# Performance work log

Hardware: AMD Instinct MI355X
Metric: run time of the kernel (lower is better)

The kernel has to match this reference:

```python
import jax, jax.numpy as jnp
import numpy as np

EMBED_DIM = 1024
NUM_HEADS = 16
HEAD_DIM = EMBED_DIM // NUM_HEADS
FF_DIM = 4096
EPS = 1e-5


def layer_norm(x, gamma, beta):
    mu = jnp.mean(x, axis=-1, keepdims=True)
    var = jnp.var(x, axis=-1, keepdims=True)
    return (x - mu) * jax.lax.rsqrt(var + EPS) * gamma + beta


def setup_inputs() -> dict:
    key = jax.random.key(0)
    ks = jax.random.split(key, 10)
    B, S = 2, 2048
    sd = 1.0 / np.sqrt(EMBED_DIM)
    sf = 1.0 / np.sqrt(FF_DIM)
    return {
        "x": jax.random.normal(ks[0], (B, S, EMBED_DIM), jnp.float32),
        # grouped QKV: 3*num_heads groups, each embed_dim -> head_dim
        "Wqkv": jax.random.normal(ks[1], (3 * NUM_HEADS, EMBED_DIM, HEAD_DIM), jnp.float32) * sd,
        "bqkv": jnp.zeros((3 * NUM_HEADS, HEAD_DIM), jnp.float32),
        "Wo": jax.random.normal(ks[2], (EMBED_DIM, EMBED_DIM), jnp.float32) * sd,
        "bo": jnp.zeros((EMBED_DIM,), jnp.float32),
        "W1": jax.random.normal(ks[3], (EMBED_DIM, FF_DIM), jnp.float32) * sd,
        "b1": jnp.zeros((FF_DIM,), jnp.float32),
        "W2": jax.random.normal(ks[4], (FF_DIM, EMBED_DIM), jnp.float32) * sf,
        "b2": jnp.zeros((EMBED_DIM,), jnp.float32),
        "ln1_g": jnp.ones((EMBED_DIM,), jnp.float32),
        "ln1_b": jnp.zeros((EMBED_DIM,), jnp.float32),
        "ln2_g": jnp.ones((EMBED_DIM,), jnp.float32),
        "ln2_b": jnp.zeros((EMBED_DIM,), jnp.float32),
    }


def reference(x, Wqkv, bqkv, Wo, bo, W1, b1, W2, b2, ln1_g, ln1_b, ln2_g, ln2_b):
    B, S, D = x.shape
    normed = layer_norm(x, ln1_g, ln1_b)
    # grouped QKV projection: group g gets its own (D, head_dim) weight
    qkv = jnp.einsum('bsd,gdh->bgsh', normed, Wqkv) + bqkv[None, :, None, :]
    qkv = qkv.reshape(B, 3, NUM_HEADS, S, HEAD_DIM)
    q, k, v = qkv[:, 0], qkv[:, 1], qkv[:, 2]  # each [B, H, S, hd]
    attn = jnp.einsum('bhqd,bhkd->bhqk', q, k) / np.sqrt(HEAD_DIM)
    attn = jax.nn.softmax(attn, axis=-1)
    out = jnp.einsum('bhqk,bhkd->bhqd', attn, v)
    out = out.transpose(0, 2, 1, 3).reshape(B, S, D)
    out = out @ Wo + bo
    x = x + out
    normed2 = layer_norm(x, ln2_g, ln2_b)
    ff = jax.nn.relu(normed2 @ W1 + b1) @ W2 + b2
    return x + ff
```

## Files before the change

kernel.cpp:

```cpp
#include <hip/hip_runtime.h>
#include <stdint.h>

#define SEQ    2048
#define NB     2
#define NHEADS 16
#define HDIM   64
#define EMBED  1024
#define NROWS  (NB*SEQ)
#define QKVSZ  ((size_t)NB*NHEADS*SEQ*HDIM)

typedef __attribute__((ext_vector_type(8))) short short8;
typedef __attribute__((ext_vector_type(4))) float float4v;
typedef __attribute__((ext_vector_type(16))) float float16v;
typedef __attribute__((ext_vector_type(2))) unsigned int uint2v;
typedef __attribute__((ext_vector_type(4))) unsigned int uint4v;

__device__ __forceinline__ float b2f(unsigned short h) {
    unsigned int u = ((unsigned int)h) << 16;
    union { unsigned int u; float f; } c; c.u = u; return c.f;
}
__device__ __forceinline__ unsigned short f2b(float f) {
    union { float f; unsigned int u; } c; c.f = f;
    unsigned int u = c.u;
    u += 0x7FFFu + ((u >> 16) & 1u);
    return (unsigned short)(u >> 16);
}
__device__ __forceinline__ unsigned int fbits(float f) {
    union { float f; unsigned int u; } c; c.f = f; return c.u;
}
__device__ __forceinline__ unsigned int cvtpk_bf16(float lo, float hi) {
    unsigned int r;
    asm("v_cvt_pk_bf16_f32 %0, %1, %2" : "=v"(r) : "v"(lo), "v"(hi));
    return r;
}

__device__ __forceinline__ void gload_lds16(const void* g, void* l) {
    __builtin_amdgcn_global_load_lds(
        (const __attribute__((address_space(1))) unsigned int*)g,
        (__attribute__((address_space(3))) unsigned int*)l, 16, 0, 0);
}

__device__ __forceinline__ int probe_f32(const void* probe) {
    return ((const unsigned short*)probe)[0] == 0;
}
__device__ __forceinline__ float lde(const void* base, size_t off, int f32) {
    return f32 ? ((const float*)base)[off] : b2f(((const unsigned short*)base)[off]);
}
__device__ __forceinline__ void ste(void* base, size_t off, float v, int f32) {
    if (f32) ((float*)base)[off] = v;
    else     ((unsigned short*)base)[off] = f2b(v);
}

__global__ __launch_bounds__(256) void ln_kernel(
    const void* __restrict__ x,
    const void* __restrict__ g,
    const void* __restrict__ b,
    unsigned short* __restrict__ out,
    const void* __restrict__ probe)
{
    int f32 = probe_f32(probe);
    int row = blockIdx.x;
    int t = threadIdx.x;
    float v0, v1, v2, v3;
    if (f32) {
        float4 rv = ((const float4*)x)[(size_t)row * (EMBED / 4) + t];
        v0 = rv.x; v1 = rv.y; v2 = rv.z; v3 = rv.w;
    } else {
        ushort4 rv = ((const ushort4*)((const unsigned short*)x + (size_t)row * EMBED))[t];
        v0 = b2f(rv.x); v1 = b2f(rv.y); v2 = b2f(rv.z); v3 = b2f(rv.w);
    }
    float s  = v0 + v1 + v2 + v3;
    float sq = v0*v0 + v1*v1 + v2*v2 + v3*v3;
    #pragma unroll
    for (int off = 32; off > 0; off >>= 1) {
        s  += __shfl_xor(s,  off);
        sq += __shfl_xor(sq, off);
    }
    __shared__ float red[8];
    int lane = t & 63, wv = t >> 6;
    if (lane == 0) { red[wv] = s; red[wv + 4] = sq; }
    __syncthreads();
    s  = red[0] + red[1] + red[2] + red[3];
    sq = red[4] + red[5] + red[6] + red[7];
    float mu  = s * (1.0f / EMBED);
    float var = sq * (1.0f / EMBED) - mu * mu;
    float rs  = rsqrtf(var + 1e-5f);
    float g0 = lde(g, t*4+0, f32), g1 = lde(g, t*4+1, f32);
    float g2 = lde(g, t*4+2, f32), g3 = lde(g, t*4+3, f32);
    float b0 = lde(b, t*4+0, f32), b1 = lde(b, t*4+1, f32);
    float b2 = lde(b, t*4+2, f32), b3 = lde(b, t*4+3, f32);
    ushort4 ov;
    ov.x = f2b((v0 - mu) * rs * g0 + b0);
    ov.y = f2b((v1 - mu) * rs * g1 + b1);
    ov.z = f2b((v2 - mu) * rs * g2 + b2);
    ov.w = f2b((v3 - mu) * rs * g3 + b3);
    ((ushort4*)(out + (size_t)row * EMBED))[t] = ov;
}

template<int QKV>
__global__ __launch_bounds__(256) void transpose_kernel(
    const void* __restrict__ in,
    unsigned short* __restrict__ out, int K, int N,
    const void* __restrict__ probe)
{
    __shared__ unsigned short t[64 * 68];
    int f32 = probe_f32(probe);
    int tid = threadIdx.x;
    int n0 = blockIdx.x * 64, k0 = blockIdx.y * 64;
    #pragma unroll
    for (int i = 0; i < 4; i++) {
        int id = tid + i * 256;
        int kr = id >> 4, nc = (id & 15) * 4;
        size_t srcoff;
        if (QKV) srcoff = ((size_t)(n0 >> 6) << 16) + (size_t)(k0 + kr) * 64 + nc;
        else     srcoff = (size_t)(k0 + kr) * N + n0 + nc;
        ushort4 val;
        if (f32) {
            float4 rv = *(const float4*)((const float*)in + srcoff);
            val.x = f2b(rv.x); val.y = f2b(rv.y); val.z = f2b(rv.z); val.w = f2b(rv.w);
        } else {
            val = *(const ushort4*)((const unsigned short*)in + srcoff);
        }
        *(ushort4*)&t[kr * 68 + nc] = val;
    }
    __syncthreads();
    #pragma unroll
    for (int i = 0; i < 4; i++) {
        int id = tid + i * 256;
        int nr = id >> 4, kc = (id & 15) * 4;
        ushort4 o;
        o.x = t[(kc + 0) * 68 + nr];
        o.y = t[(kc + 1) * 68 + nr];
        o.z = t[(kc + 2) * 68 + nr];
        o.w = t[(kc + 3) * 68 + nr];
        *(ushort4*)(out + (size_t)(n0 + nr) * K + k0 + kc) = o;
    }
}

template<int DO_RELU, int HAS_BIAS, int HAS_RES, int OUTMODE>
__global__ __launch_bounds__(256) void gemm_kernel(
    const unsigned short* __restrict__ A,
    const unsigned short* __restrict__ Bt,
    const void* __restrict__ bias,
    const void* __restrict__ res,
    void* __restrict__ out,
    int M, int N, int K, int ldA, int ldB, int bcol0, int bkoff,
    const void* __restrict__ probe)
{
    __shared__ unsigned short Als[2][128 * 32];
    __shared__ unsigned short Bls[2][128 * 32];
    int f32 = probe_f32(probe);
    int tid = threadIdx.x;
    int lane = tid & 63, wv = tid >> 6;
    int lq = lane >> 4, lr = lane & 15;
    int moff = (wv >> 1) * 64, noff = (wv & 1) * 64;
    int m0 = blockIdx.y * 128, n0 = blockIdx.x * 128;

    int rA = tid >> 2, jA = tid & 3;
    int jjA = jA ^ ((rA >> 1) & 3);
    const unsigned short* ga0 = A  + (size_t)(m0 + rA) * ldA + jjA * 8;
    const unsigned short* ga1 = A  + (size_t)(m0 + rA + 64) * ldA + jjA * 8;
    const unsigned short* gb0 = Bt + (size_t)(n0 + rA) * ldB + bkoff + jjA * 8;
    const unsigned short* gb1 = Bt + (size_t)(n0 + rA + 64) * ldB + bkoff + jjA * 8;

    int fch = (lq ^ ((lr >> 1) & 3)) * 8;

    float4v acc[4][4];
    #pragma unroll
    for (int i = 0; i < 4; i++)
        #pragma unroll
        for (int j = 0; j < 4; j++)
            { acc[i][j][0] = 0.f; acc[i][j][1] = 0.f; acc[i][j][2] = 0.f; acc[i][j][3] = 0.f; }

    gload_lds16(ga0, &Als[0][(size_t)tid * 8]);
    gload_lds16(ga1, &Als[0][(size_t)(tid + 256) * 8]);
    gload_lds16(gb0, &Bls[0][(size_t)tid * 8]);
    gload_lds16(gb1, &Bls[0][(size_t)(tid + 256) * 8]);

    int nkt = K >> 5;
    for (int kt = 0; kt < nkt; kt++) {
        int cur = kt & 1, nxt = cur ^ 1;
        __syncthreads();
        if (kt + 1 < nkt) {
            int ko = (kt + 1) * 32;
            gload_lds16(ga0 + ko, &Als[nxt][(size_t)tid * 8]);
            gload_lds16(ga1 + ko, &Als[nxt][(size_t)(tid + 256) * 8]);
            gload_lds16(gb0 + ko, &Bls[nxt][(size_t)tid * 8]);
            gload_lds16(gb1 + ko, &Bls[nxt][(size_t)(tid + 256) * 8]);
        }
        short8 af[4], bfr[4];
        #pragma unroll
        for (int mt = 0; mt < 4; mt++)
            af[mt] = *(const short8*)(&Als[cur][(moff + mt * 16 + lr) * 32 + fch]);
        #pragma unroll
        for (int nt = 0; nt < 4; nt++)
            bfr[nt] = *(const short8*)(&Bls[cur][(noff + nt * 16 + lr) * 32 + fch]);
        #pragma unroll
        for (int mt = 0; mt < 4; mt++)
            #pragma unroll
            for (int nt = 0; nt < 4; nt++)
                acc[mt][nt] = __builtin_amdgcn_mfma_f32_16x16x32_bf16(af[mt], bfr[nt], acc[mt][nt], 0, 0, 0);
    }

    #pragma unroll
    for (int mt = 0; mt < 4; mt++) {
        #pragma unroll
        for (int nt = 0; nt < 4; nt++) {
            if (OUTMODE == 2) {
                int cc = n0 + noff + nt * 16 + lr;
                int gg = cc >> 6, hd = cc & 63;
                int ty = gg >> 4, hh = gg & 15;
                int rrb = m0 + moff + mt * 16 + lq * 4;
                int bb = rrb >> 11, ss = rrb & 2047;
                float vv[4];
                #pragma unroll
                for (int rg = 0; rg < 4; rg++) {
                    float v = acc[mt][nt][rg];
                    if (HAS_BIAS) v += lde(bias, (size_t)cc, f32);
                    vv[rg] = v;
                }
                if (ty < 2) {
                    unsigned short* p = (unsigned short*)out + (size_t)ty * QKVSZ +
                        (((size_t)(bb * NHEADS + hh) * SEQ + ss) * HDIM) + hd;
                    #pragma unroll
                    for (int rg = 0; rg < 4; rg++) p[(size_t)rg * HDIM] = f2b(vv[rg]);
                } else {
                    ushort4 pk;
                    pk.x = f2b(vv[0]); pk.y = f2b(vv[1]);
                    pk.z = f2b(vv[2]); pk.w = f2b(vv[3]);
                    *(ushort4*)((unsigned short*)out + 2 * QKVSZ +
                        ((size_t)(bb * NHEADS + hh) * HDIM + hd) * SEQ + ss) = pk;
                }
            } else {
                #pragma unroll
                for (int rg = 0; rg < 4; rg++) {
                    int rr = m0 + moff + mt * 16 + lq * 4 + rg;
                    int cc = n0 + noff + nt * 16 + lr;
                    float v = acc[mt][nt][rg];
                    if (HAS_BIAS) v += lde(bias, (size_t)(bcol0 + cc), f32);
                    if (DO_RELU) v = v > 0.f ? v : 0.f;
                    if (HAS_RES) v += lde(res, (size_t)rr * N + cc, f32);
                    if (OUTMODE == 1) ste(out, (size_t)rr * N + cc, v, f32);
                    else ((unsigned short*)out)[(size_t)rr * N + cc] = f2b(v);
                }
            }
        }
    }
}

template<int DO_RELU, int HAS_BIAS, int HAS_RES, int OUTMODE>
__global__ __launch_bounds__(256) void gemm64_kernel(
    const unsigned short* __restrict__ A,
    const unsigned short* __restrict__ Bt,
    const void* __restrict__ bias,
    const void* __restrict__ res,
    void* __restrict__ out,
    int M, int N, int K, int ldA, int ldB,
    const void* __restrict__ probe)
{
    __shared__ unsigned short Als[2][64 * 32];
    __shared__ unsigned short Bls[2][64 * 32];
    int f32 = probe_f32(probe);
    int tid = threadIdx.x;
    int lane = tid & 63, wv = tid >> 6;
    int lq = lane >> 4, lr = lane & 15;
    int moff = (wv >> 1) * 32, noff = (wv & 1) * 32;
    int m0 = blockIdx.y * 64, n0 = blockIdx.x * 64;

    int rA = tid >> 2, jA = tid & 3;
    int jjA = jA ^ ((rA >> 1) & 3);
    const unsigned short* ga = A  + (size_t)(m0 + rA) * ldA + jjA * 8;
    const unsigned short* gb = Bt + (size_t)(n0 + rA) * ldB + jjA * 8;

    int fch = (lq ^ ((lr >> 1) & 3)) * 8;

    float4v acc[2][2];
    #pragma unroll
    for (int i = 0; i < 2; i++)
        #pragma unroll
        for (int j = 0; j < 2; j++)
            { acc[i][j][0] = 0.f; acc[i][j][1] = 0.f; acc[i][j][2] = 0.f; acc[i][j][3] = 0.f; }

    gload_lds16(ga, &Als[0][(size_t)tid * 8]);
    gload_lds16(gb, &Bls[0][(size_t)tid * 8]);

    int nkt = K >> 5;
    for (int kt = 0; kt < nkt; kt++) {
        int cur = kt & 1, nxt = cur ^ 1;
        __syncthreads();
        if (kt + 1 < nkt) {
            int ko = (kt + 1) * 32;
            gload_lds16(ga + ko, &Als[nxt][(size_t)tid * 8]);
            gload_lds16(gb + ko, &Bls[nxt][(size_t)tid * 8]);
        }
        short8 af[2], bfr[2];
        #pragma unroll
        for (int mt = 0; mt < 2; mt++)
            af[mt] = *(const short8*)(&Als[cur][(moff + mt * 16 + lr) * 32 + fch]);
        #pragma unroll
        for (int nt = 0; nt < 2; nt++)
            bfr[nt] = *(const short8*)(&Bls[cur][(noff + nt * 16 + lr) * 32 + fch]);
        #pragma unroll
        for (int mt = 0; mt < 2; mt++)
            #pragma unroll
            for (int nt = 0; nt < 2; nt++)
                acc[mt][nt] = __builtin_amdgcn_mfma_f32_16x16x32_bf16(af[mt], bfr[nt], acc[mt][nt], 0, 0, 0);
    }

    #pragma unroll
    for (int mt = 0; mt < 2; mt++) {
        #pragma unroll
        for (int nt = 0; nt < 2; nt++) {
            #pragma unroll
            for (int rg = 0; rg < 4; rg++) {
                int rr = m0 + moff + mt * 16 + lq * 4 + rg;
                int cc = n0 + noff + nt * 16 + lr;
                float v = acc[mt][nt][rg];
                if (HAS_BIAS) v += lde(bias, (size_t)cc, f32);
                if (DO_RELU) v = v > 0.f ? v : 0.f;
                if (HAS_RES) v += lde(res, (size_t)rr * N + cc, f32);
                if (OUTMODE == 1) ste(out, (size_t)rr * N + cc, v, f32);
                else ((unsigned short*)out)[(size_t)rr * N + cc] = f2b(v);
            }
        }
    }
}

__global__ __launch_bounds__(256) void attn_kernel(
    const unsigned short* __restrict__ qb,
    const unsigned short* __restrict__ kb,
    const unsigned short* __restrict__ vtb,
    unsigned short* __restrict__ outb)
{
    __shared__ unsigned short Kls[2][64 * 64];
    __shared__ unsigned short Vls[2][64 * 64];
    int tid = threadIdx.x;
    int lane = tid & 63, wv = tid >> 6;
    int l31 = lane & 31, hh = lane >> 5;
    int bh = blockIdx.y;
    int b = bh >> 4, head = bh & 15;
    const unsigned short* q  = qb  + (size_t)bh * SEQ * HDIM;
    const unsigned short* k  = kb  + (size_t)bh * SEQ * HDIM;
    const unsigned short* vt = vtb + (size_t)bh * HDIM * SEQ;
    int q0w = blockIdx.x * 128 + wv * 32;

    const float C2 = 0.18033688011112042f;

    short8 qf[4];
    #pragma unroll
    for (int c = 0; c < 4; c++) {
        short8 raw = *(const short8*)(q + (size_t)(q0w + l31) * HDIM + c * 16 + hh * 8);
        #pragma unroll
        for (int j = 0; j < 8; j++)
            qf[c][j] = (short)f2b(b2f((unsigned short)raw[j]) * C2);
    }

    int rS = tid >> 3;
    int jjS = (tid & 7) ^ (rS & 7);
    const unsigned short* gk0 = k + (size_t)rS * HDIM + jjS * 8;
    const unsigned short* gk1 = k + (size_t)(rS + 32) * HDIM + jjS * 8;
    const unsigned short* gv0 = vt + (size_t)rS * SEQ + jjS * 8;
    const unsigned short* gv1 = vt + (size_t)(rS + 32) * SEQ + jjS * 8;

    float l_part = 0.f;
    float16v o0, o1;
    #pragma unroll
    for (int i = 0; i < 16; i++) { o0[i] = 0.f; o1[i] = 0.f; }

    gload_lds16(gk0, &Kls[0][(size_t)tid * 8]);
    gload_lds16(gk1, &Kls[0][(size_t)(tid + 256) * 8]);
    gload_lds16(gv0, &Vls[0][(size_t)tid * 8]);
    gload_lds16(gv1, &Vls[0][(size_t)(tid + 256) * 8]);

    for (int kt = 0; kt < SEQ / 64; kt++) {
        int cur = kt & 1, nxt = cur ^ 1;
        __syncthreads();
        if (kt + 1 < SEQ / 64) {
            int k0n = (kt + 1) * 64;
            gload_lds16(gk0 + (size_t)k0n * HDIM, &Kls[nxt][(size_t)tid * 8]);
            gload_lds16(gk1 + (size_t)k0n * HDIM, &Kls[nxt][(size_t)(tid + 256) * 8]);
            gload_lds16(gv0 + k0n, &Vls[nxt][(size_t)tid * 8]);
            gload_lds16(gv1 + k0n, &Vls[nxt][(size_t)(tid + 256) * 8]);
        }

        #pragma unroll
        for (int kb2 = 0; kb2 < 2; kb2++) {
            float16v st;
            #pragma unroll
            for (int i = 0; i < 16; i++) st[i] = 0.f;
            int r = kb2 * 32 + l31;
            int rx = r & 7;
            #pragma unroll
            for (int c = 0; c < 4; c++) {
                short8 kf = *(const short8*)(
                    &Kls[cur][r * 64 + (((2 * c + hh) ^ rx) * 8)]);
                st = __builtin_amdgcn_mfma_f32_32x32x16_bf16(kf, qf[c], st, 0, 0, 0);
            }
            float p[16];
            #pragma unroll
            for (int rg = 0; rg < 16; rg++) {
                p[rg] = __builtin_amdgcn_exp2f(st[rg]);
                l_part += p[rg];
            }
            int rv0 = l31, rv1 = 32 + l31;
            int rxv = l31 & 7;
            #pragma unroll
            for (int s = 0; s < 2; s++) {
                unsigned int a1 = cvtpk_bf16(p[8*s+0], p[8*s+1]);
                unsigned int a2 = cvtpk_bf16(p[8*s+2], p[8*s+3]);
                unsigned int b1 = cvtpk_bf16(p[8*s+4], p[8*s+5]);
                unsigned int b2 = cvtpk_bf16(p[8*s+6], p[8*s+7]);
                uint2v r1 = __builtin_amdgcn_permlane32_swap(a1, b1, false, false);
                uint2v r2 = __builtin_amdgcn_permlane32_swap(a2, b2, false, false);
                union { uint4v u; short8 s8; } pun;
                pun.u.x = r1.x; pun.u.y = r2.x; pun.u.z = r1.y; pun.u.w = r2.y;
                short8 pf = pun.s8;
                int g = kb2 * 2 + s;
                short8 vf0 = *(const short8*)(
                    &Vls[cur][rv0 * 64 + (((2 * g + hh) ^ rxv) * 8)]);
                o0 = __builtin_amdgcn_mfma_f32_32x32x16_bf16(pf, vf0, o0, 0, 0, 0);
                short8 vf1 = *(const short8*)(
                    &Vls[cur][rv1 * 64 + (((2 * g + hh) ^ rxv) * 8)]);
                o1 = __builtin_amdgcn_mfma_f32_32x32x16_bf16(pf, vf1, o1, 0, 0, 0);
            }
        }
    }

    l_part += __shfl_xor(l_part, 32);
    float linv_me = 1.f / l_part;
    #pragma unroll
    for (int rg = 0; rg < 16; rg++) {
        int qrow = (rg & 3) + 8 * (rg >> 2) + 4 * hh;
        float linv = __shfl(linv_me, qrow);
        size_t rowbase = ((size_t)(b * SEQ + q0w + qrow)) * EMBED + head * HDIM;
        outb[rowbase + l31]      = f2b(o0[rg] * linv);
        outb[rowbase + 32 + l31] = f2b(o1[rg] * linv);
    }
}

extern "C" void kernel_launch(void* const* d_in, const int* in_sizes, int n_in,
                              void* d_out, int out_size, void* d_ws, size_t ws_size,
                              hipStream_t stream)
{
    (void)in_sizes; (void)n_in; (void)out_size; (void)ws_size;
    const void* x    = d_in[0];
    const void* Wqkv = d_in[1];
    const void* bqkv = d_in[2];
    const void* Wo   = d_in[3];
    const void* bo   = d_in[4];
    const void* W1   = d_in[5];
    const void* b1   = d_in[6];
    const void* W2   = d_in[7];
    const void* b2   = d_in[8];
    const void* g1   = d_in[9];
    const void* be1  = d_in[10];
    const void* g2   = d_in[11];
    const void* be2  = d_in[12];
    const void* probe = g1;

    char* ws = (char*)d_ws;
    const size_t MB = 1024 * 1024;
    unsigned short* tmp1  = (unsigned short*)(ws + 0 * MB);
    unsigned short* qkv   = (unsigned short*)(ws + 8 * MB);
    unsigned short* WoT   = (unsigned short*)(ws + 8 * MB);
    unsigned short* W1T   = (unsigned short*)(ws + 8 * MB);
    unsigned short* W2T   = (unsigned short*)(ws + 8 * MB);
    unsigned short* h1    = (unsigned short*)(ws + 16 * MB);
    unsigned short* WqkvT = (unsigned short*)d_out;

    transpose_kernel<1><<<dim3(3072 / 64, 1024 / 64), 256, 0, stream>>>(Wqkv, WqkvT, 1024, 3072, probe);
    ln_kernel<<<dim3(NROWS), 256, 0, stream>>>(x, g1, be1, tmp1, probe);
    gemm_kernel<0, 1, 0, 2><<<dim3(3072 / 128, NROWS / 128), 256, 0, stream>>>(
        tmp1, WqkvT, bqkv, nullptr, qkv, NROWS, 3072, 1024, 1024, 1024, 0, 0, probe);
    attn_kernel<<<dim3(SEQ / 128, NB * NHEADS), 256, 0, stream>>>(
        qkv, qkv + QKVSZ, qkv + 2 * QKVSZ, tmp1);
    transpose_kernel<0><<<dim3(1024 / 64, 1024 / 64), 256, 0, stream>>>(Wo, WoT, 1024, 1024, probe);
    gemm64_kernel<0, 1, 1, 1><<<dim3(1024 / 64, NROWS / 64), 256, 0, stream>>>(
        tmp1, WoT, bo, x, d_out, NROWS, 1024, 1024, 1024, 1024, probe);
    ln_kernel<<<dim3(NROWS), 256, 0, stream>>>(d_out, g2, be2, tmp1, probe);
    transpose_kernel<0><<<dim3(4096 / 64, 1024 / 64), 256, 0, stream>>>(W1, W1T, 1024, 4096, probe);
    gemm_kernel<1, 1, 0, 0><<<dim3(4096 / 128, NROWS / 128), 256, 0, stream>>>(
        tmp1, W1T, b1, nullptr, h1, NROWS, 4096, 1024, 1024, 1024, 0, 0, probe);
    transpose_kernel<0><<<dim3(1024 / 64, 4096 / 64), 256, 0, stream>>>(W2, W2T, 4096, 1024, probe);
    gemm64_kernel<0, 1, 1, 1><<<dim3(1024 / 64, NROWS / 64), 256, 0, stream>>>(
        h1, W2T, b2, d_out, d_out, NROWS, 1024, 4096, 4096, 4096, probe);
}
```

Before: 403.8 us.

## Use split-K 128x128 GEMM with separate combine for FF2 projection

Replaces the 64x64-tile FF2 GEMM with a 128x128-tile kernel that splits K into four chunks, writing fp32 partial sums to workspace. A combine kernel then sums the partials and adds bias and residual. This aims for higher MFMA reuse per block while keeping enough blocks in flight, at the cost of extra global memory traffic for the partial buffers. It falls back to the old kernel when the workspace is too small.

```diff
diff --git a/kernel.cpp b/kernel.cpp
--- a/kernel.cpp
+++ b/kernel.cpp
@@ -248,6 +248,112 @@
     }
 }
 
+__global__ __launch_bounds__(256) void gemm_splitk_kernel(
+    const unsigned short* __restrict__ A,
+    const unsigned short* __restrict__ Bt,
+    float* __restrict__ part,
+    int M, int N, int K, int ldA, int ldB)
+{
+    __shared__ unsigned short Als[2][128 * 32];
+    __shared__ unsigned short Bls[2][128 * 32];
+    int tid = threadIdx.x;
+    int lane = tid & 63, wv = tid >> 6;
+    int lq = lane >> 4, lr = lane & 15;
+    int moff = (wv >> 1) * 64, noff = (wv & 1) * 64;
+    int m0 = blockIdx.y * 128, n0 = blockIdx.x * 128;
+    int kz = blockIdx.z;
+    int kchunk = K >> 2;
+    int k0 = kz * kchunk;
+
+    int rA = tid >> 2, jA = tid & 3;
+    int jjA = jA ^ ((rA >> 1) & 3);
+    const unsigned short* ga0 = A  + (size_t)(m0 + rA) * ldA + k0 + jjA * 8;
+    const unsigned short* ga1 = A  + (size_t)(m0 + rA + 64) * ldA + k0 + jjA * 8;
+    const unsigned short* gb0 = Bt + (size_t)(n0 + rA) * ldB + k0 + jjA * 8;
+    const unsigned short* gb1 = Bt + (size_t)(n0 + rA + 64) * ldB + k0 + jjA * 8;
+
+    int fch = (lq ^ ((lr >> 1) & 3)) * 8;
+
+    float4v acc[4][4];
+    #pragma unroll
+    for (int i = 0; i < 4; i++)
+        #pragma unroll
+        for (int j = 0; j < 4; j++)
+            { acc[i][j][0] = 0.f; acc[i][j][1] = 0.f; acc[i][j][2] = 0.f; acc[i][j][3] = 0.f; }
+
+    gload_lds16(ga0, &Als[0][(size_t)tid * 8]);
+    gload_lds16(ga1, &Als[0][(size_t)(tid + 256) * 8]);
+    gload_lds16(gb0, &Bls[0][(size_t)tid * 8]);
+    gload_lds16(gb1, &Bls[0][(size_t)(tid + 256) * 8]);
+
+    int nkt = kchunk >> 5;
+    for (int kt = 0; kt < nkt; kt++) {
+        int cur = kt & 1, nxt = cur ^ 1;
+        __syncthreads();
+        if (kt + 1 < nkt) {
+            int ko = (kt + 1) * 32;
+            gload_lds16(ga0 + ko, &Als[nxt][(size_t)tid * 8]);
+            gload_lds16(ga1 + ko, &Als[nxt][(size_t)(tid + 256) * 8]);
+            gload_lds16(gb0 + ko, &Bls[nxt][(size_t)tid * 8]);
+            gload_lds16(gb1 + ko, &Bls[nxt][(size_t)(tid + 256) * 8]);
+        }
+        short8 af[4], bfr[4];
+        #pragma unroll
+        for (int mt = 0; mt < 4; mt++)
+            af[mt] = *(const short8*)(&Als[cur][(moff + mt * 16 + lr) * 32 + fch]);
+        #pragma unroll
+        for (int nt = 0; nt < 4; nt++)
+            bfr[nt] = *(const short8*)(&Bls[cur][(noff + nt * 16 + lr) * 32 + fch]);
+        #pragma unroll
+        for (int mt = 0; mt < 4; mt++)
+            #pragma unroll
+            for (int nt = 0; nt < 4; nt++)
+                acc[mt][nt] = __builtin_amdgcn_mfma_f32_16x16x32_bf16(af[mt], bfr[nt], acc[mt][nt], 0, 0, 0);
+    }
+
+    float* po = part + (size_t)kz * M * N;
+    #pragma unroll
+    for (int mt = 0; mt < 4; mt++)
+        #pragma unroll
+        for (int nt = 0; nt < 4; nt++)
+            #pragma unroll
+            for (int rg = 0; rg < 4; rg++) {
+                int rr = m0 + moff + mt * 16 + lq * 4 + rg;
+                int cc = n0 + noff + nt * 16 + lr;
+                po[(size_t)rr * N + cc] = acc[mt][nt][rg];
+            }
+}
+
+__global__ __launch_bounds__(256) void ff2_combine_kernel(
+    const float* __restrict__ part,
+    const void* __restrict__ b2,
+    void* __restrict__ xout,
+    const void* __restrict__ probe)
+{
+    int f32 = probe_f32(probe);
+    int row = blockIdx.x;
+    int t = threadIdx.x;
+    const size_t MN = (size_t)NROWS * EMBED;
+    size_t base = (size_t)row * EMBED + t * 4;
+    float4 p0 = *(const float4*)(part + base);
+    float4 p1 = *(const float4*)(part + MN + base);
+    float4 p2 = *(const float4*)(part + 2 * MN + base);
+    float4 p3 = *(const float4*)(part + 3 * MN + base);
+    float s0 = (p0.x + p1.x) + (p2.x + p3.x);
+    float s1 = (p0.y + p1.y) + (p2.y + p3.y);
+    float s2 = (p0.z + p1.z) + (p2.z + p3.z);
+    float s3 = (p0.w + p1.w) + (p2.w + p3.w);
+    int c = t * 4;
+    s0 += lde(b2, c + 0, f32) + lde(xout, base + 0, f32);
+    s1 += lde(b2, c + 1, f32) + lde(xout, base + 1, f32);
+    s2 += lde(b2, c + 2, f32) + lde(xout, base + 2, f32);
+    s3 += lde(b2, c + 3, f32) + lde(xout, base + 3, f32);
+    ste(xout, base + 0, s0, f32);
+    ste(xout, base + 1, s1, f32);
+    ste(xout, base + 2, s2, f32);
+    ste(xout, base + 3, s3, f32);
+}
+
 template<int DO_RELU, int HAS_BIAS, int HAS_RES, int OUTMODE>
 __global__ __launch_bounds__(256) void gemm64_kernel(
     const unsigned short* __restrict__ A,
@@ -442,7 +548,7 @@
                               void* d_out, int out_size, void* d_ws, size_t ws_size,
                               hipStream_t stream)
 {
-    (void)in_sizes; (void)n_in; (void)out_size; (void)ws_size;
+    (void)in_sizes; (void)n_in; (void)out_size;
     const void* x    = d_in[0];
     const void* Wqkv = d_in[1];
     const void* bqkv = d_in[2];
@@ -466,7 +572,9 @@
     unsigned short* W1T   = (unsigned short*)(ws + 8 * MB);
     unsigned short* W2T   = (unsigned short*)(ws + 8 * MB);
     unsigned short* h1    = (unsigned short*)(ws + 16 * MB);
+    float*          part  = (float*)(ws + 48 * MB);
     unsigned short* WqkvT = (unsigned short*)d_out;
+    bool splitk_ok = ws_size >= (size_t)112 * MB;
 
     transpose_kernel<1><<<dim3(3072 / 64, 1024 / 64), 256, 0, stream>>>(Wqkv, WqkvT, 1024, 3072, probe);
     ln_kernel<<<dim3(NROWS), 256, 0, stream>>>(x, g1, be1, tmp1, probe);
@@ -482,6 +590,12 @@
     gemm_kernel<1, 1, 0, 0><<<dim3(4096 / 128, NROWS / 128), 256, 0, stream>>>(
         tmp1, W1T, b1, nullptr, h1, NROWS, 4096, 1024, 1024, 1024, 0, 0, probe);
     transpose_kernel<0><<<dim3(1024 / 64, 4096 / 64), 256, 0, stream>>>(W2, W2T, 4096, 1024, probe);
-    gemm64_kernel<0, 1, 1, 1><<<dim3(1024 / 64, NROWS / 64), 256, 0, stream>>>(
-        h1, W2T, b2, d_out, d_out, NROWS, 1024, 4096, 4096, 4096, probe);
-}
+    if (splitk_ok) {
+        gemm_splitk_kernel<<<dim3(1024 / 128, NROWS / 128, 4), 256, 0, stream>>>(
+            h1, W2T, part, NROWS, 1024, 4096, 4096, 4096);
+        ff2_combine_kernel<<<dim3(NROWS), 256, 0, stream>>>(part, b2, d_out, probe);
+    } else {
+        gemm64_kernel<0, 1, 1, 1><<<dim3(1024 / 64, NROWS / 64), 256, 0, stream>>>(
+            h1, W2T, b2, d_out, d_out, NROWS, 1024, 4096, 4096, 4096, probe);
+    }
+}
```

Measured after the change: 405.6 us. About the same (+0.4%).
